# Performance work log

Hardware: AMD Instinct MI355X
Metric: run time of the kernel (lower is better)

Reference implementation:

```python
import jax, jax.numpy as jnp
import numpy as np

N_INPUT = 4096
N_NEURONS = 4096
T = 500
DT = 1.0
RATE = 0.05  # Bernoulli input spike probability per timestep

# LIF constants (Diehl&Cook-style excitatory / inhibitory populations)
E_REST, E_RESET, E_THRESH, E_TAU, E_REFRAC = -65.0, -65.0, -52.0, 100.0, 5.0
I_REST, I_RESET, I_THRESH, I_TAU, I_REFRAC = -60.0, -45.0, -40.0, 10.0, 2.0


def setup_inputs() -> dict:
    key = jax.random.key(0)
    k1, k2 = jax.random.split(key, 2)
    # Input group spike train: [T, n_input] of {0,1} floats (Poisson-like)
    inpts_X = (jax.random.uniform(k1, (T, N_INPUT)) < RATE).astype(jnp.float32)
    # X -> Ae learned weights (positive, small)
    w_xe = jax.random.uniform(k2, (N_INPUT, N_NEURONS), dtype=jnp.float32) * 0.3
    eye = jnp.eye(N_NEURONS, dtype=jnp.float32)
    # Ae -> Ai: one-to-one excitation; Ai -> Ae: all-but-self inhibition
    w_ei = 22.5 * eye
    w_ie = -17.5 * (1.0 - eye)
    return {"inpts_X": inpts_X, "w_xe": w_xe, "w_ei": w_ei, "w_ie": w_ie, "time": T}


def _lif(v, rc, inpt, rest, reset, thresh, tau, refrac):
    # Integrate only outside refractory period
    active = (rc <= 0).astype(v.dtype)
    v = v + (DT / tau) * (rest - v) + active * inpt
    rc = jnp.maximum(rc - DT, 0.0)
    s = (v >= thresh).astype(v.dtype)
    rc = jnp.where(s > 0, refrac, rc)
    v = jnp.where(s > 0, reset, v)
    return v, rc, s


def reference(inpts_X, w_xe, w_ei, w_ie, time):
    n_x = inpts_X.shape[1]
    n_e = w_xe.shape[1]
    n_i = w_ei.shape[1]
    f32 = inpts_X.dtype

    def step(carry, x_t):
        s_x, v_e, rc_e, s_e, v_i, rc_i, s_i = carry
        # get_inputs(): messages use spikes from the END of the previous step
        in_e = s_x @ w_xe + s_i @ w_ie   # inputs to excitatory group
        in_i = s_e @ w_ei                # inputs to inhibitory group
        s_x_new = x_t                    # InputGroup: s = current input row
        v_e2, rc_e2, s_e2 = _lif(v_e, rc_e, in_e, E_REST, E_RESET, E_THRESH, E_TAU, E_REFRAC)
        v_i2, rc_i2, s_i2 = _lif(v_i, rc_i, in_i, I_REST, I_RESET, I_THRESH, I_TAU, I_REFRAC)
        new_carry = (s_x_new, v_e2, rc_e2, s_e2, v_i2, rc_i2, s_i2)
        return new_carry, (s_x_new, s_e2, s_i2)

    init = (
        jnp.zeros((n_x,), f32),
        jnp.full((n_e,), E_REST, f32), jnp.zeros((n_e,), f32), jnp.zeros((n_e,), f32),
        jnp.full((n_i,), I_REST, f32), jnp.zeros((n_i,), f32), jnp.zeros((n_i,), f32),
    )
    _, (sx, se, si) = jax.lax.scan(step, init, inpts_X[: int(time)])
    # spikes dict -> concatenated [T, n_x + n_e + n_i]
    return jnp.concatenate([sx, se, si], axis=1)
```

## Files before the change

### kernel.cpp

```cpp
#include <hip/hip_runtime.h>

#define N 4096
#define OUTW 12288

__global__ void compact_spikes(const float* __restrict__ X, int* __restrict__ idx,
                               int* __restrict__ cnt, float* __restrict__ out, int T) {
    int t = blockIdx.x;
    const float* row = X + (size_t)t * N;
    __shared__ int counts[256];
    int tid = threadIdx.x;
    int base = tid * 16;
    float4 r0 = *(const float4*)(row + base);
    float4 r1 = *(const float4*)(row + base + 4);
    float4 r2 = *(const float4*)(row + base + 8);
    float4 r3 = *(const float4*)(row + base + 12);
    float* orow = out + (size_t)t * OUTW + base;
    *(float4*)(orow)      = r0;
    *(float4*)(orow + 4)  = r1;
    *(float4*)(orow + 8)  = r2;
    *(float4*)(orow + 12) = r3;
    float vals[16];
    *(float4*)(vals)      = r0;
    *(float4*)(vals + 4)  = r1;
    *(float4*)(vals + 8)  = r2;
    *(float4*)(vals + 12) = r3;
    int ks[16];
    int c = 0;
    #pragma unroll
    for (int q = 0; q < 16; ++q) {
        if (vals[q] != 0.0f) ks[c++] = base + q;
    }
    counts[tid] = c;
    __syncthreads();
    int off = 0;
    for (int i = 0; i < tid; ++i) off += counts[i];
    int* op = idx + (size_t)t * N;
    for (int q = 0; q < c; ++q) op[off + q] = ks[q];
    if (tid == 255) cnt[t] = off + c;
}

__global__ void __launch_bounds__(1024)
fused(const float* __restrict__ W, const int* __restrict__ idx,
      const int* __restrict__ cnt, float* __restrict__ XW,
      unsigned char* __restrict__ pk, float* __restrict__ state,
      int ra, int rb, int ca, int cb, int T) {
    __shared__ int sidx[4096];
    __shared__ unsigned int cS[3];
    const int tid = threadIdx.x;

    if (blockIdx.x == 0) {
        if (ca >= cb) return;
        const int lane = tid & 63;
        float ve[4], ref[4];
        unsigned int R, E, zp;
        unsigned char pw;
        float* st = state + (size_t)tid * 12;
        if (ca == 0) {
            #pragma unroll
            for (int q = 0; q < 4; ++q) { ve[q] = -65.0f; ref[q] = 0.0f; }
            R = 0u; E = 0u; zp = 0u; pw = 0;
            if (tid == 0) { cS[0] = 0u; cS[1] = 0u; cS[2] = 0u; }
        } else {
            float4 a = *(float4*)(st);
            float4 b = *(float4*)(st + 4);
            uint4  c = *(uint4*)(st + 8);
            ve[0] = a.x; ve[1] = a.y; ve[2] = a.z; ve[3] = a.w;
            ref[0] = b.x; ref[1] = b.y; ref[2] = b.z; ref[3] = b.w;
            R = c.x; E = c.y; zp = c.z; pw = (unsigned char)c.w;
            if (tid == 0) {
                cS[0] = 0u; cS[1] = 0u;
                cS[2] = *(unsigned int*)(state + 12 * 1024);
            }
        }
        const float4* xwp = (const float4*)XW + tid;
        float4 xw = xwp[(size_t)ca * 1024];
        unsigned char* pkp = pk + tid;
        int prev = 2, cur = 0, nxt = 1;
        __syncthreads();

        for (int t = ca; t < cb; ++t) {
            unsigned int Sint = cS[prev];
            if (t > 0) pkp[(size_t)(t - 1) * 1024] = pw;
            float4 xw_n = xw;
            if (t + 1 < cb) xw_n = xwp[(size_t)(t + 1) * 1024];
            if (tid == 0) cS[nxt] = 0u;
            unsigned int nz = (R | (R >> 1)) & 0x01010101u;
            unsigned int z  = (nz ^ 0x01010101u) & E;
            R = (R - nz) | (z << 1);
            int c0 = __popcll(__ballot((z & 0x000000ffu) != 0u));
            int c1 = __popcll(__ballot((z & 0x0000ff00u) != 0u));
            int c2 = __popcll(__ballot((z & 0x00ff0000u) != 0u));
            int c3 = __popcll(__ballot((z & 0xff000000u) != 0u));
            if (lane == 0) atomicAdd(&cS[cur], (unsigned int)(c0 + c1 + c2 + c3));
            float Sf  = (float)Sint;
            float Sf1 = Sf - 1.0f;
            const float xq[4] = {xw.x, xw.y, xw.z, xw.w};
            unsigned int sbits = 0u;
            #pragma unroll
            for (int q = 0; q < 4; ++q) {
                unsigned int bq = (zp >> (q * 8)) & 1u;
                float dS = bq ? Sf1 : Sf;
                float in_e = xq[q] - 17.5f * dS;
                float in_sel = (ref[q] <= 0.0f) ? in_e : 0.0f;
                float v = ve[q] + 0.01f * (-65.0f - ve[q]) + in_sel;
                float rc = fmaxf(ref[q] - 1.0f, 0.0f);
                int s = (v >= -52.0f) ? 1 : 0;
                ref[q] = s ? 5.0f : rc;
                ve[q]  = s ? -65.0f : v;
                sbits |= (unsigned int)s << q;
            }
            E = (sbits * 0x00204081u) & 0x01010101u;
            unsigned int znib = (z * 0x10204080u) >> 24;
            pw = (unsigned char)(sbits | znib);
            zp = z;
            xw = xw_n;
            int tmp = prev; prev = cur; cur = nxt; nxt = tmp;
            __syncthreads();
        }
        pkp[(size_t)(cb - 1) * 1024] = pw;
        if (cb < T) {
            float4 a = {ve[0], ve[1], ve[2], ve[3]};
            float4 b = {ref[0], ref[1], ref[2], ref[3]};
            uint4  c = {R, E, zp, (unsigned int)pw};
            *(float4*)(st)     = a;
            *(float4*)(st + 4) = b;
            *(uint4*)(st + 8)  = c;
            if (tid == 0) *(unsigned int*)(state + 12 * 1024) = cS[prev];
        }
        return;
    }

    int b = (int)blockIdx.x - 1;
    int r = ra + (b >> 1);
    int half = b & 1;
    if (r >= rb) return;
    float4 acc = {0.f, 0.f, 0.f, 0.f};
    int col = (half << 11) + ((tid & 511) << 2);
    if (r > 0) {
        int c = cnt[r - 1];
        const int* ip = idx + (size_t)(r - 1) * N;
        for (int s = tid; s < c; s += 1024) sidx[s] = ip[s];
        __syncthreads();
        if (tid < 512) {
            const float* Wc = W + col;
            int s = 0;
            for (; s + 8 <= c; s += 8) {
                float4 w0 = *(const float4*)(Wc + (size_t)sidx[s]     * N);
                float4 w1 = *(const float4*)(Wc + (size_t)sidx[s + 1] * N);
                float4 w2 = *(const float4*)(Wc + (size_t)sidx[s + 2] * N);
                float4 w3 = *(const float4*)(Wc + (size_t)sidx[s + 3] * N);
                float4 w4 = *(const float4*)(Wc + (size_t)sidx[s + 4] * N);
                float4 w5 = *(const float4*)(Wc + (size_t)sidx[s + 5] * N);
                float4 w6 = *(const float4*)(Wc + (size_t)sidx[s + 6] * N);
                float4 w7 = *(const float4*)(Wc + (size_t)sidx[s + 7] * N);
                acc.x += w0.x; acc.y += w0.y; acc.z += w0.z; acc.w += w0.w;
                acc.x += w1.x; acc.y += w1.y; acc.z += w1.z; acc.w += w1.w;
                acc.x += w2.x; acc.y += w2.y; acc.z += w2.z; acc.w += w2.w;
                acc.x += w3.x; acc.y += w3.y; acc.z += w3.z; acc.w += w3.w;
                acc.x += w4.x; acc.y += w4.y; acc.z += w4.z; acc.w += w4.w;
                acc.x += w5.x; acc.y += w5.y; acc.z += w5.z; acc.w += w5.w;
                acc.x += w6.x; acc.y += w6.y; acc.z += w6.z; acc.w += w6.w;
                acc.x += w7.x; acc.y += w7.y; acc.z += w7.z; acc.w += w7.w;
            }
            for (; s < c; ++s) {
                float4 w0 = *(const float4*)(Wc + (size_t)sidx[s] * N);
                acc.x += w0.x; acc.y += w0.y; acc.z += w0.z; acc.w += w0.w;
            }
        }
    }
    if (tid < 512) *(float4*)(XW + (size_t)r * N + col) = acc;
}

__global__ void expand(const unsigned char* __restrict__ pk, float* __restrict__ out, int T) {
    int i = blockIdx.x * 256 + threadIdx.x;
    if (i >= T * 1024) return;
    int t = i >> 10;
    int g = i & 1023;
    unsigned int b = pk[i];
    float* orow = out + (size_t)t * OUTW + N + (size_t)g * 4;
    float4 se4 = {(float)(b & 1u), (float)((b >> 1) & 1u),
                  (float)((b >> 2) & 1u), (float)((b >> 3) & 1u)};
    float4 si4 = {(float)((b >> 4) & 1u), (float)((b >> 5) & 1u),
                  (float)((b >> 6) & 1u), (float)((b >> 7) & 1u)};
    *(float4*)orow = se4;
    *(float4*)(orow + N) = si4;
}

extern "C" void kernel_launch(void* const* d_in, const int* in_sizes, int n_in,
                              void* d_out, int out_size, void* d_ws, size_t ws_size,
                              hipStream_t stream) {
    const float* X   = (const float*)d_in[0];
    const float* Wxe = (const float*)d_in[1];
    int T = in_sizes[0] / N;
    float* out = (float*)d_out;

    float* XW = (float*)d_ws;
    int* idx  = (int*)((char*)d_ws + (size_t)T * N * 4);
    int* cnt  = (int*)((char*)d_ws + (size_t)2 * T * N * 4);
    unsigned char* pk = (unsigned char*)idx;
    float* state = (float*)((char*)idx + 40 * 16384);

    compact_spikes<<<T, 256, 0, stream>>>(X, idx, cnt, out, T);

    const int C = 100;
    int nch = (T + C - 1) / C;
    for (int i = 0; i <= nch; ++i) {
        int ra = i * C, rb = (i + 1) * C;
        if (ra > T) ra = T;
        if (rb > T) rb = T;
        int ca = (i - 1) * C, cb = i * C;
        if (ca < 0) ca = 0;
        if (cb > T) cb = T;
        if (i == 0) { ca = cb = 0; }
        int grid = 1 + 2 * (rb - ra);
        fused<<<grid, 1024, 0, stream>>>(Wxe, idx, cnt, XW, pk, state,
                                         ra, rb, ca, cb, T);
    }

    expand<<<(T * 1024 + 255) / 256, 256, 0, stream>>>(pk, out, T);
}
```

Measured before the change: 487.7 us.

## Remap spike-gather blocks to 8 rows per block and shrink last pipeline chunk

The sparse input-weight gather blocks are reorganised so each 1024-thread block handles 8 timestep rows, each across a 512-column slice. All threads are now active, instead of half sitting idle, and shared index storage is capped at 512 entries per row, with a global-memory fallback beyond that. The host chunking also changes: the last chunk is shortened to 20 rows, so the final serial LIF chunk that cannot overlap any gather work is smaller. This trades weight-row locality across column halves for better thread utilisation and less serial tail time.

```diff
diff --git a/kernel.cpp b/kernel.cpp
--- a/kernel.cpp
+++ b/kernel.cpp
@@ -44,7 +44,6 @@
       const int* __restrict__ cnt, float* __restrict__ XW,
       unsigned char* __restrict__ pk, float* __restrict__ state,
       int ra, int rb, int ca, int cb, int T) {
-    __shared__ int sidx[4096];
     __shared__ unsigned int cS[3];
     const int tid = threadIdx.x;
 
@@ -130,45 +129,59 @@
         return;
     }
 
+    __shared__ int sidx[8][512];
     int b = (int)blockIdx.x - 1;
-    int r = ra + (b >> 1);
-    int half = b & 1;
-    if (r >= rb) return;
+    int s8 = b & 7;
+    int p  = b >> 3;
+    int g  = tid >> 7;
+    int ln = tid & 127;
+    int r  = ra + 8 * p + g;
+    int valid = (r < rb);
+    int c = 0;
+    const int* ip = nullptr;
+    if (valid && r > 0) {
+        c = cnt[r - 1];
+        ip = idx + (size_t)(r - 1) * N;
+        int lim = c < 512 ? c : 512;
+        for (int j = ln; j < lim; j += 128) sidx[g][j] = ip[j];
+    }
+    __syncthreads();
+    if (!valid) return;
+    int col = (s8 << 9) + (ln << 2);
     float4 acc = {0.f, 0.f, 0.f, 0.f};
-    int col = (half << 11) + ((tid & 511) << 2);
     if (r > 0) {
-        int c = cnt[r - 1];
-        const int* ip = idx + (size_t)(r - 1) * N;
-        for (int s = tid; s < c; s += 1024) sidx[s] = ip[s];
-        __syncthreads();
-        if (tid < 512) {
-            const float* Wc = W + col;
-            int s = 0;
-            for (; s + 8 <= c; s += 8) {
-                float4 w0 = *(const float4*)(Wc + (size_t)sidx[s]     * N);
-                float4 w1 = *(const float4*)(Wc + (size_t)sidx[s + 1] * N);
-                float4 w2 = *(const float4*)(Wc + (size_t)sidx[s + 2] * N);
-                float4 w3 = *(const float4*)(Wc + (size_t)sidx[s + 3] * N);
-                float4 w4 = *(const float4*)(Wc + (size_t)sidx[s + 4] * N);
-                float4 w5 = *(const float4*)(Wc + (size_t)sidx[s + 5] * N);
-                float4 w6 = *(const float4*)(Wc + (size_t)sidx[s + 6] * N);
-                float4 w7 = *(const float4*)(Wc + (size_t)sidx[s + 7] * N);
-                acc.x += w0.x; acc.y += w0.y; acc.z += w0.z; acc.w += w0.w;
-                acc.x += w1.x; acc.y += w1.y; acc.z += w1.z; acc.w += w1.w;
-                acc.x += w2.x; acc.y += w2.y; acc.z += w2.z; acc.w += w2.w;
-                acc.x += w3.x; acc.y += w3.y; acc.z += w3.z; acc.w += w3.w;
-                acc.x += w4.x; acc.y += w4.y; acc.z += w4.z; acc.w += w4.w;
-                acc.x += w5.x; acc.y += w5.y; acc.z += w5.z; acc.w += w5.w;
-                acc.x += w6.x; acc.y += w6.y; acc.z += w6.z; acc.w += w6.w;
-                acc.x += w7.x; acc.y += w7.y; acc.z += w7.z; acc.w += w7.w;
-            }
-            for (; s < c; ++s) {
-                float4 w0 = *(const float4*)(Wc + (size_t)sidx[s] * N);
-                acc.x += w0.x; acc.y += w0.y; acc.z += w0.z; acc.w += w0.w;
-            }
-        }
-    }
-    if (tid < 512) *(float4*)(XW + (size_t)r * N + col) = acc;
+        const float* Wc = W + col;
+        const int* sg = sidx[g];
+        int lim = c < 512 ? c : 512;
+        int s = 0;
+        for (; s + 8 <= lim; s += 8) {
+            float4 w0 = *(const float4*)(Wc + (size_t)sg[s]     * N);
+            float4 w1 = *(const float4*)(Wc + (size_t)sg[s + 1] * N);
+            float4 w2 = *(const float4*)(Wc + (size_t)sg[s + 2] * N);
+            float4 w3 = *(const float4*)(Wc + (size_t)sg[s + 3] * N);
+            float4 w4 = *(const float4*)(Wc + (size_t)sg[s + 4] * N);
+            float4 w5 = *(const float4*)(Wc + (size_t)sg[s + 5] * N);
+            float4 w6 = *(const float4*)(Wc + (size_t)sg[s + 6] * N);
+            float4 w7 = *(const float4*)(Wc + (size_t)sg[s + 7] * N);
+            acc.x += w0.x; acc.y += w0.y; acc.z += w0.z; acc.w += w0.w;
+            acc.x += w1.x; acc.y += w1.y; acc.z += w1.z; acc.w += w1.w;
+            acc.x += w2.x; acc.y += w2.y; acc.z += w2.z; acc.w += w2.w;
+            acc.x += w3.x; acc.y += w3.y; acc.z += w3.z; acc.w += w3.w;
+            acc.x += w4.x; acc.y += w4.y; acc.z += w4.z; acc.w += w4.w;
+            acc.x += w5.x; acc.y += w5.y; acc.z += w5.z; acc.w += w5.w;
+            acc.x += w6.x; acc.y += w6.y; acc.z += w6.z; acc.w += w6.w;
+            acc.x += w7.x; acc.y += w7.y; acc.z += w7.z; acc.w += w7.w;
+        }
+        for (; s < lim; ++s) {
+            float4 w0 = *(const float4*)(Wc + (size_t)sg[s] * N);
+            acc.x += w0.x; acc.y += w0.y; acc.z += w0.z; acc.w += w0.w;
+        }
+        for (; s < c; ++s) {
+            float4 w0 = *(const float4*)(Wc + (size_t)ip[s] * N);
+            acc.x += w0.x; acc.y += w0.y; acc.z += w0.z; acc.w += w0.w;
+        }
+    }
+    *(float4*)(XW + (size_t)r * N + col) = acc;
 }
 
 __global__ void expand(const unsigned char* __restrict__ pk, float* __restrict__ out, int T) {
@@ -202,17 +215,23 @@
 
     compact_spikes<<<T, 256, 0, stream>>>(X, idx, cnt, out, T);
 
-    const int C = 100;
-    int nch = (T + C - 1) / C;
+    int bounds[16];
+    int nb = 0;
+    bounds[nb++] = 0;
+    if (T >= 140) {
+        for (int x = 100; x <= T - 140; x += 100) bounds[nb++] = x;
+        bounds[nb++] = T - 20;
+    }
+    bounds[nb++] = T;
+    int nch = nb - 1;
+
     for (int i = 0; i <= nch; ++i) {
-        int ra = i * C, rb = (i + 1) * C;
-        if (ra > T) ra = T;
-        if (rb > T) rb = T;
-        int ca = (i - 1) * C, cb = i * C;
-        if (ca < 0) ca = 0;
-        if (cb > T) cb = T;
-        if (i == 0) { ca = cb = 0; }
-        int grid = 1 + 2 * (rb - ra);
+        int ra = (i < nch) ? bounds[i] : T;
+        int rb = (i < nch) ? bounds[i + 1] : T;
+        int ca = (i >= 1) ? bounds[i - 1] : 0;
+        int cb = (i >= 1) ? bounds[i] : 0;
+        int nrow = rb - ra;
+        int grid = 1 + 8 * ((nrow + 7) / 8);
         fused<<<grid, 1024, 0, stream>>>(Wxe, idx, cnt, XW, pk, state,
                                          ra, rb, ca, cb, T);
     }
```

New measurement: 463.4 us. 1.05x faster.
